# Kernel tuning notes

Hardware: AMD Instinct MI355X
Metric: run time of the kernel (lower is better)

## Reference

```python
import jax, jax.numpy as jnp
import numpy as np

N, E, B, IN, DIM, H = 20000, 320000, 128, 25, 64, 8

def _lin(key, fin, fout):
    k1, k2 = jax.random.split(key)
    s = 1.0 / np.sqrt(fin)
    return (jax.random.uniform(k1, (fin, fout), jnp.float32, -s, s),
            jax.random.uniform(k2, (fout,), jnp.float32, -s, s))

def setup_inputs() -> dict:
    key = jax.random.key(0)
    ks = jax.random.split(key, 12)
    x = jax.random.normal(ks[0], (N, IN), jnp.float32)
    edge_index = jax.random.randint(ks[1], (2, E), 0, N, jnp.int64)
    batch = jnp.sort(jax.random.randint(ks[2], (N,), 0, B, jnp.int64))
    W0, b0 = _lin(ks[3], IN, DIM)
    Wg, _ = _lin(ks[4], DIM, H * DIM)            # GATConv lin (no bias)
    att_src = jax.random.normal(ks[5], (H, DIM), jnp.float32) * (1.0 / np.sqrt(DIM))
    att_dst = jax.random.normal(ks[6], (H, DIM), jnp.float32) * (1.0 / np.sqrt(DIM))
    bg = jnp.zeros((H * DIM,), jnp.float32)       # GATConv output bias
    Wh, bh = _lin(ks[7], H * DIM, DIM)            # head_nn
    sl = 1.0 / np.sqrt(DIM)
    W_ih = jax.random.uniform(ks[8], (4 * DIM, 2 * DIM), jnp.float32, -sl, sl)
    W_hh = jax.random.uniform(ks[9], (4 * DIM, DIM), jnp.float32, -sl, sl)
    b_ih = jnp.zeros((4 * DIM,), jnp.float32)
    b_hh = jnp.zeros((4 * DIM,), jnp.float32)
    W1, b1 = _lin(ks[10], 2 * DIM, DIM)
    W2, b2 = _lin(ks[11], DIM, 1)
    return dict(x=x, edge_index=edge_index, batch=batch, W0=W0, b0=b0, Wg=Wg,
                att_src=att_src, att_dst=att_dst, bg=bg, Wh=Wh, bh=bh,
                W_ih=W_ih, W_hh=W_hh, b_ih=b_ih, b_hh=b_hh, W1=W1, b1=b1, W2=W2, b2=b2)

def _forward(x, edge_index, batch, W0, b0, Wg, att_src, att_dst, bg, Wh, bh,
             W_ih, W_hh, b_ih, b_hh, W1, b1, W2, b2):
    n = x.shape[0]
    h0 = jax.nn.relu(x @ W0 + b0)                         # [N, DIM]
    xh = (h0 @ Wg).reshape(n, H, DIM)                     # [N, H, C]
    # add self-loops (PyG GATConv default)
    loop = jnp.arange(n, dtype=edge_index.dtype)
    src = jnp.concatenate([edge_index[0], loop])
    dst = jnp.concatenate([edge_index[1], loop])
    a_s = jnp.einsum('nhc,hc->nh', xh, att_src)           # [N, H]
    a_d = jnp.einsum('nhc,hc->nh', xh, att_dst)
    e = jax.nn.leaky_relu(a_s[src] + a_d[dst], 0.2)       # [Etot, H]
    m = jax.ops.segment_max(e, dst, num_segments=n)
    w = jnp.exp(e - m[dst])
    s = jax.ops.segment_sum(w, dst, num_segments=n)
    alpha = w / s[dst]                                    # segment softmax over dst
    agg = jax.ops.segment_sum(alpha[:, :, None] * xh[src], dst, num_segments=n)
    out = jax.nn.relu(agg.reshape(n, H * DIM) + bg)
    out = jax.nn.relu(out @ Wh + bh)                      # [N, DIM]
    # Set2Set, 3 processing steps
    q_star = jnp.zeros((B, 2 * DIM), out.dtype)
    h = jnp.zeros((B, DIM), out.dtype)
    c = jnp.zeros((B, DIM), out.dtype)
    for _ in range(3):
        g = q_star @ W_ih.T + b_ih + h @ W_hh.T + b_hh
        i_g, f_g, g_g, o_g = jnp.split(g, 4, axis=-1)
        c = jax.nn.sigmoid(f_g) * c + jax.nn.sigmoid(i_g) * jnp.tanh(g_g)
        h = jax.nn.sigmoid(o_g) * jnp.tanh(c)
        q = h                                             # [B, DIM]
        e2 = jnp.sum(out * q[batch], axis=-1)             # [N]
        m2 = jax.ops.segment_max(e2, batch, num_segments=B)
        w2 = jnp.exp(e2 - m2[batch])
        s2 = jax.ops.segment_sum(w2, batch, num_segments=B)
        a2 = w2 / s2[batch]
        r = jax.ops.segment_sum(a2[:, None] * out, batch, num_segments=B)
        q_star = jnp.concatenate([q, r], axis=-1)
    y = jax.nn.relu(q_star @ W1 + b1)
    y = y @ W2 + b2
    return y.reshape(-1)

def reference(x, edge_index, batch, W0, b0, Wg, att_src, att_dst, bg, Wh, bh,
              W_ih, W_hh, b_ih, b_hh, W1, b1, W2, b2):
    return _forward(x, edge_index, batch, W0, b0, Wg, att_src, att_dst, bg, Wh, bh,
                    W_ih, W_hh, b_ih, b_hh, W1, b1, W2, b2)
```

## Files before the change

kernel.cpp:

```cpp
#include <hip/hip_runtime.h>

#define N_NODES 20000
#define N_EDGES 320000
#define NBATCH  128

__device__ __forceinline__ float lrelu(float v) { return v > 0.f ? v : 0.2f * v; }

__global__ void k_h0(const float* __restrict__ x, const float* __restrict__ W0,
                     const float* __restrict__ b0, float* __restrict__ h0,
                     int* __restrict__ deg, int n) {
    __shared__ float ws[25 * 64];
    __shared__ float bs[64];
    __shared__ float xs[100];
    int t = threadIdx.x;
    int gid = blockIdx.x * 256 + t;
    if (gid < n) deg[gid] = 0;
    for (int i = t; i < 25 * 64; i += 256) ws[i] = W0[i];
    if (t < 64) bs[t] = b0[t];
    int nb = blockIdx.x * 4;
    if (t < 100 && nb * 25 + t < n * 25) xs[t] = x[(size_t)nb * 25 + t];
    __syncthreads();
    int node = nb + (t >> 6);
    int c = t & 63;
    if (node >= n) return;
    float s = bs[c];
    const float* xr = xs + (t >> 6) * 25;
    #pragma unroll
    for (int k = 0; k < 25; k++) s += xr[k] * ws[k * 64 + c];
    h0[(size_t)node * 64 + c] = fmaxf(s, 0.f);
}

__global__ void k_small(const float* __restrict__ Wg, const float* __restrict__ att_s,
                        const float* __restrict__ att_d, float* __restrict__ vsd,
                        const int* __restrict__ batch, int* __restrict__ segst, int n, int b) {
    int t = threadIdx.x;
    if (blockIdx.x == 0) {
        int k = t >> 3, h = t & 7;
        const float* wrow = Wg + (size_t)k * 512 + h * 64;
        float s1 = 0.f, s2 = 0.f;
        #pragma unroll 8
        for (int c = 0; c < 64; c++) {
            float w = wrow[c];
            s1 += w * att_s[h * 64 + c];
            s2 += w * att_d[h * 64 + c];
        }
        vsd[k * 16 + h] = s1;
        vsd[k * 16 + 8 + h] = s2;
    } else {
        if (t > b) return;
        int lo = 0, hi = n;
        while (lo < hi) { int mid = (lo + hi) >> 1; if (batch[mid] < t) lo = mid + 1; else hi = mid; }
        segst[t] = lo;
    }
}

__global__ __launch_bounds__(256) void k_asd(const float* __restrict__ h0,
                                             const float* __restrict__ vsd,
                                             float* __restrict__ a_s, float* __restrict__ a_d) {
    __shared__ float hs[16][65];
    __shared__ float vl[64 * 16];
    int tid = threadIdx.x;
    int rbase = blockIdx.x * 16;
    {
        int row = tid / 16, c4 = (tid % 16) * 4;
        float4 hv = *(const float4*)(h0 + (size_t)(rbase + row) * 64 + c4);
        hs[row][c4] = hv.x; hs[row][c4 + 1] = hv.y; hs[row][c4 + 2] = hv.z; hs[row][c4 + 3] = hv.w;
    }
    #pragma unroll
    for (int j = 0; j < 4; j++) vl[tid + j * 256] = vsd[tid + j * 256];
    __syncthreads();
    int nl = tid / 16, o = tid % 16;
    float acc = 0.f;
    #pragma unroll 16
    for (int k = 0; k < 64; k++) acc += hs[nl][k] * vl[k * 16 + o];
    int node = rbase + nl;
    if (o < 8) a_s[node * 8 + o] = acc;
    else       a_d[node * 8 + (o - 8)] = acc;
}

__global__ void k_count(const int* __restrict__ dst, int* __restrict__ deg, int e) {
    int i = blockIdx.x * 256 + threadIdx.x;
    if (i < e) atomicAdd(&deg[dst[i]], 1);
}

__global__ __launch_bounds__(1024) void k_scan1(const int* __restrict__ deg,
                                                int* __restrict__ tmp, int* __restrict__ bsum, int n) {
    __shared__ int wsum[16];
    int tid = threadIdx.x, lane = tid & 63, w = tid >> 6;
    int i = blockIdx.x * 1024 + tid;
    int v = (i < n) ? deg[i] + 1 : 0;
    int x = v;
    #pragma unroll
    for (int off = 1; off < 64; off <<= 1) {
        int t = __shfl_up(x, off);
        if (lane >= off) x += t;
    }
    if (lane == 63) wsum[w] = x;
    __syncthreads();
    int pre = 0;
    #pragma unroll
    for (int j = 0; j < 16; j++) if (j < w) pre += wsum[j];
    if (i < n) tmp[i] = pre + x - v;
    if (tid == 1023) bsum[blockIdx.x] = pre + x;
}

__global__ void k_scan2(const int* __restrict__ tmp, const int* __restrict__ bsum,
                        const float* __restrict__ a_s, const float* __restrict__ a_d,
                        int* __restrict__ offs, int* __restrict__ adj,
                        int* __restrict__ cursor, float* __restrict__ eb, int n, int nblk) {
    int i = blockIdx.x * 256 + threadIdx.x;
    if (i > n) return;
    int b = i >> 10;
    int pre = 0;
    for (int j = 0; j < b; j++) pre += bsum[j];
    if (i == n) {
        int tot = pre;
        for (int j = b; j < nblk; j++) tot += bsum[j];
        offs[n] = tot;
        return;
    }
    int o = pre + tmp[i];
    offs[i] = o;
    adj[o] = i;
    cursor[i] = o + 1;
    float4 s0 = *(const float4*)(a_s + (size_t)i * 8);
    float4 s1 = *(const float4*)(a_s + (size_t)i * 8 + 4);
    float4 d0 = *(const float4*)(a_d + (size_t)i * 8);
    float4 d1 = *(const float4*)(a_d + (size_t)i * 8 + 4);
    float4 e0, e1;
    e0.x = lrelu(s0.x + d0.x); e0.y = lrelu(s0.y + d0.y);
    e0.z = lrelu(s0.z + d0.z); e0.w = lrelu(s0.w + d0.w);
    e1.x = lrelu(s1.x + d1.x); e1.y = lrelu(s1.y + d1.y);
    e1.z = lrelu(s1.z + d1.z); e1.w = lrelu(s1.w + d1.w);
    *(float4*)(eb + (size_t)o * 8) = e0;
    *(float4*)(eb + (size_t)o * 8 + 4) = e1;
}

__global__ void k_fill_edge(const int* __restrict__ src, const int* __restrict__ dst,
                            const float* __restrict__ a_s, const float* __restrict__ a_d,
                            int* __restrict__ cursor, int* __restrict__ adj,
                            float* __restrict__ eb, int e) {
    int i = blockIdx.x * 256 + threadIdx.x;
    if (i >= e) return;
    int s = src[i], d = dst[i];
    int p = atomicAdd(&cursor[d], 1);
    adj[p] = s;
    float4 s0 = *(const float4*)(a_s + (size_t)s * 8);
    float4 s1 = *(const float4*)(a_s + (size_t)s * 8 + 4);
    float4 d0 = *(const float4*)(a_d + (size_t)d * 8);
    float4 d1 = *(const float4*)(a_d + (size_t)d * 8 + 4);
    float4 e0, e1;
    e0.x = lrelu(s0.x + d0.x); e0.y = lrelu(s0.y + d0.y);
    e0.z = lrelu(s0.z + d0.z); e0.w = lrelu(s0.w + d0.w);
    e1.x = lrelu(s1.x + d1.x); e1.y = lrelu(s1.y + d1.y);
    e1.z = lrelu(s1.z + d1.z); e1.w = lrelu(s1.w + d1.w);
    *(float4*)(eb + (size_t)p * 8) = e0;
    *(float4*)(eb + (size_t)p * 8 + 4) = e1;
}

__global__ __launch_bounds__(256) void k_gat3(const int* __restrict__ offs, const int* __restrict__ adj,
                                              const float* __restrict__ eb,
                                              const float* __restrict__ h0,
                                              float* __restrict__ agg_pre, int n) {
    int lane = threadIdx.x & 63;
    int node = blockIdx.x * 4 + (threadIdx.x >> 6);
    if (node >= n) return;
    int beg = offs[node], end = offs[node + 1];
    int g = lane >> 3;

    float m = -1e30f, s = 0.f;
    for (int base = beg; base < end; base += 8) {
        if (base + g < end) {
            float ev = eb[(size_t)base * 8 + lane];
            if (ev > m) { s = s * __expf(m - ev) + 1.f; m = ev; }
            else        { s += __expf(ev - m); }
        }
    }
    #pragma unroll
    for (int off = 8; off < 64; off <<= 1) {
        float mo = __shfl_xor(m, off), so = __shfl_xor(s, off);
        float mn = fmaxf(m, mo);
        s = s * __expf(m - mn) + so * __expf(mo - mn);
        m = mn;
    }
    float rcp = 1.f / s;

    float acc[8] = {0.f, 0.f, 0.f, 0.f, 0.f, 0.f, 0.f, 0.f};
    for (int sbase = beg; sbase < end; sbase += 64) {
        int scnt = end - sbase; if (scnt > 64) scnt = 64;
        int srcv = 0;
        if (lane < scnt) srcv = adj[sbase + lane];
        float al[8];
        #pragma unroll
        for (int j = 0; j < 8; j++) {
            int q = j * 8 + g;
            float ev = -1e30f;
            if (q < scnt) ev = eb[(size_t)sbase * 8 + j * 64 + lane];
            al[j] = __expf(ev - m) * rcp;
        }
        for (int j = 0; j < 8; j++) {
            int qb = j * 8;
            if (qb >= scnt) break;
            int sg[8]; float xv[8];
            #pragma unroll
            for (int g2 = 0; g2 < 8; g2++) sg[g2] = __shfl(srcv, qb + g2);
            #pragma unroll
            for (int g2 = 0; g2 < 8; g2++)
                xv[g2] = h0[(size_t)sg[g2] * 64 + lane];
            #pragma unroll
            for (int g2 = 0; g2 < 8; g2++) {
                #pragma unroll
                for (int h2 = 0; h2 < 8; h2++)
                    acc[h2] += __shfl(al[j], g2 * 8 + h2) * xv[g2];
            }
        }
    }
    #pragma unroll
    for (int h2 = 0; h2 < 8; h2++)
        agg_pre[(size_t)node * 512 + h2 * 64 + lane] = acc[h2];
}

__global__ __launch_bounds__(256) void k_fused3(const float* __restrict__ agg_pre,
                                                const float* __restrict__ Wg,
                                                const float* __restrict__ bg,
                                                const float* __restrict__ Wh,
                                                float* __restrict__ part, int M) {
    __shared__ float As[64 * 68];
    __shared__ float Bs[64 * 64];
    __shared__ float Cs[64 * 68];
    int tid = threadIdx.x;
    int r0 = blockIdx.x * 64;
    int tx = tid % 16, ty = tid / 16;
    int rr = tid / 16, c4 = (tid % 16) * 4;
    float accO[4][4] = {};
    #pragma unroll
    for (int hh = 0; hh < 2; hh++) {
        int h = blockIdx.y * 2 + hh;
        #pragma unroll
        for (int pp = 0; pp < 4; pp++) {
            int r = rr + pp * 16;
            float4 av = make_float4(0.f, 0.f, 0.f, 0.f);
            if (r0 + r < M) av = *(const float4*)(agg_pre + (size_t)(r0 + r) * 512 + h * 64 + c4);
            *(float4*)&As[r * 68 + c4] = av;
            *(float4*)&Bs[r * 64 + c4] = *(const float4*)(Wg + (size_t)r * 512 + h * 64 + c4);
        }
        __syncthreads();
        float acc1[4][4] = {};
        #pragma unroll 4
        for (int kc = 0; kc < 16; kc++) {
            float4 b0 = *(const float4*)&Bs[(kc * 4 + 0) * 64 + tx * 4];
            float4 b1 = *(const float4*)&Bs[(kc * 4 + 1) * 64 + tx * 4];
            float4 b2 = *(const float4*)&Bs[(kc * 4 + 2) * 64 + tx * 4];
            float4 b3 = *(const float4*)&Bs[(kc * 4 + 3) * 64 + tx * 4];
            #pragma unroll
            for (int i = 0; i < 4; i++) {
                float4 a = *(const float4*)&As[(ty * 4 + i) * 68 + kc * 4];
                acc1[i][0] += a.x * b0.x + a.y * b1.x + a.z * b2.x + a.w * b3.x;
                acc1[i][1] += a.x * b0.y + a.y * b1.y + a.z * b2.y + a.w * b3.y;
                acc1[i][2] += a.x * b0.z + a.y * b1.z + a.z * b2.z + a.w * b3.z;
                acc1[i][3] += a.x * b0.w + a.y * b1.w + a.z * b2.w + a.w * b3.w;
            }
        }
        __syncthreads();
        float4 bgv = *(const float4*)(bg + h * 64 + tx * 4);
        #pragma unroll
        for (int i = 0; i < 4; i++) {
            float4 o;
            o.x = fmaxf(acc1[i][0] + bgv.x, 0.f);
            o.y = fmaxf(acc1[i][1] + bgv.y, 0.f);
            o.z = fmaxf(acc1[i][2] + bgv.z, 0.f);
            o.w = fmaxf(acc1[i][3] + bgv.w, 0.f);
            *(float4*)&Cs[(ty * 4 + i) * 68 + tx * 4] = o;
        }
        #pragma unroll
        for (int pp = 0; pp < 4; pp++) {
            int k = rr + pp * 16;
            *(float4*)&Bs[k * 64 + c4] = *(const float4*)(Wh + (size_t)(h * 64 + k) * 64 + c4);
        }
        __syncthreads();
        #pragma unroll 4
        for (int kc = 0; kc < 16; kc++) {
            float4 b0 = *(const float4*)&Bs[(kc * 4 + 0) * 64 + tx * 4];
            float4 b1 = *(const float4*)&Bs[(kc * 4 + 1) * 64 + tx * 4];
            float4 b2 = *(const float4*)&Bs[(kc * 4 + 2) * 64 + tx * 4];
            float4 b3 = *(const float4*)&Bs[(kc * 4 + 3) * 64 + tx * 4];
            #pragma unroll
            for (int i = 0; i < 4; i++) {
                float4 a = *(const float4*)&Cs[(ty * 4 + i) * 68 + kc * 4];
                accO[i][0] += a.x * b0.x + a.y * b1.x + a.z * b2.x + a.w * b3.x;
                accO[i][1] += a.x * b0.y + a.y * b1.y + a.z * b2.y + a.w * b3.y;
                accO[i][2] += a.x * b0.z + a.y * b1.z + a.z * b2.z + a.w * b3.z;
                accO[i][3] += a.x * b0.w + a.y * b1.w + a.z * b2.w + a.w * b3.w;
            }
        }
        __syncthreads();
    }
    float* Cb = part + (size_t)blockIdx.y * M * 64;
    #pragma unroll
    for (int i = 0; i < 4; i++) {
        int r = r0 + ty * 4 + i;
        if (r >= M) continue;
        float4 o;
        o.x = accO[i][0]; o.y = accO[i][1]; o.z = accO[i][2]; o.w = accO[i][3];
        *(float4*)(Cb + (size_t)r * 64 + tx * 4) = o;
    }
}

__global__ void k_reduce4(const float* __restrict__ part, const float* __restrict__ bias,
                          float* __restrict__ out, int M) {
    int idx = blockIdx.x * 256 + threadIdx.x;
    if (idx >= M * 16) return;
    int r = idx / 16, cq = idx % 16;
    float4 s = make_float4(0.f, 0.f, 0.f, 0.f);
    #pragma unroll
    for (int y = 0; y < 4; y++) {
        float4 p = *(const float4*)(part + ((size_t)y * M + r) * 64 + cq * 4);
        s.x += p.x; s.y += p.y; s.z += p.z; s.w += p.w;
    }
    float4 b = *(const float4*)(bias + cq * 4);
    s.x = fmaxf(s.x + b.x, 0.f); s.y = fmaxf(s.y + b.y, 0.f);
    s.z = fmaxf(s.z + b.z, 0.f); s.w = fmaxf(s.w + b.w, 0.f);
    *(float4*)(out + (size_t)r * 64 + cq * 4) = s;
}

#define SROWS 208
__global__ __launch_bounds__(256) void k_s2s(const float* __restrict__ out2,
                                             const int* __restrict__ segst,
                                             const float* __restrict__ W_ih, const float* __restrict__ W_hh,
                                             const float* __restrict__ b_ih, const float* __restrict__ b_hh,
                                             const float* __restrict__ W1, const float* __restrict__ b1,
                                             const float* __restrict__ W2, const float* __restrict__ b2,
                                             float* __restrict__ out) {
    int b = blockIdx.x, tid = threadIdx.x, lane = tid & 63, w = tid >> 6;
    __shared__ float sc[SROWS * 65];
    __shared__ float wlds[1024];
    __shared__ float hl[64], cl[64], rl[64];
    __shared__ float red[4];
    __shared__ float gsh[256];
    int beg = segst[b], end = segst[b + 1];
    int nrows = end - beg;
    int ncache = nrows < SROWS ? nrows : SROWS;
    for (int idx = tid; idx < ncache * 16; idx += 256) {
        int r = idx >> 4, q = idx & 15;
        float4 v = *(const float4*)(out2 + (size_t)(beg + r) * 64 + q * 4);
        float* p = &sc[r * 65 + q * 4];
        p[0] = v.x; p[1] = v.y; p[2] = v.z; p[3] = v.w;
    }
    if (tid < 64) { hl[tid] = 0.f; cl[tid] = 0.f; rl[tid] = 0.f; }
    __syncthreads();

    for (int it = 0; it < 3; it++) {
        {
            float acc = b_ih[tid] + b_hh[tid];
            const float* wi = W_ih + (size_t)tid * 128;
            const float* wh = W_hh + (size_t)tid * 64;
            #pragma unroll 8
            for (int k = 0; k < 64; k++) acc += hl[k] * (wi[k] + wh[k]) + rl[k] * wi[64 + k];
            gsh[tid] = acc;
        }
        __syncthreads();
        if (tid < 64) {
            float ig = gsh[tid], fg = gsh[64 + tid], gg = gsh[128 + tid], og = gsh[192 + tid];
            float cc = cl[tid];
            float si = 1.f / (1.f + __expf(-ig));
            float sf = 1.f / (1.f + __expf(-fg));
            float so = 1.f / (1.f + __expf(-og));
            float cn = sf * cc + si * tanhf(gg);
            cl[tid] = cn;
            hl[tid] = so * tanhf(cn);
        }
        __syncthreads();
        float ev[4];
        int nr = 0;
        float mloc = -1e30f;
        for (int i = tid; i < nrows; i += 256) {
            float d = 0.f;
            if (i < SROWS) {
                const float* rp = &sc[i * 65];
                #pragma unroll 16
                for (int j = 0; j < 64; j++) d += rp[j] * hl[j];
            } else {
                const float* rp = out2 + (size_t)(beg + i) * 64;
                for (int j = 0; j < 64; j++) d += rp[j] * hl[j];
            }
            ev[nr++] = d;
            mloc = fmaxf(mloc, d);
        }
        #pragma unroll
        for (int off = 1; off < 64; off <<= 1) mloc = fmaxf(mloc, __shfl_xor(mloc, off));
        if (lane == 0) red[w] = mloc;
        __syncthreads();
        float m = fmaxf(fmaxf(red[0], red[1]), fmaxf(red[2], red[3]));
        __syncthreads();
        float sloc = 0.f;
        nr = 0;
        for (int i = tid; i < nrows; i += 256) {
            float wv = __expf(ev[nr++] - m);
            if (i < 1024) wlds[i] = wv;
            sloc += wv;
        }
        #pragma unroll
        for (int off = 1; off < 64; off <<= 1) sloc += __shfl_xor(sloc, off);
        if (lane == 0) red[w] = sloc;
        __syncthreads();
        float sv = red[0] + red[1] + red[2] + red[3];
        float inv = sv > 0.f ? 1.f / sv : 0.f;
        float acc = 0.f;
        for (int i = w; i < nrows; i += 4) {
            float v = (i < SROWS) ? sc[i * 65 + lane] : out2[(size_t)(beg + i) * 64 + lane];
            acc += wlds[i] * v;
        }
        gsh[w * 64 + lane] = acc;
        __syncthreads();
        if (tid < 64)
            rl[tid] = (gsh[tid] + gsh[64 + tid] + gsh[128 + tid] + gsh[192 + tid]) * inv;
        __syncthreads();
    }
    if (tid < 64) {
        float t = b1[tid];
        #pragma unroll 8
        for (int k = 0; k < 64; k++)
            t += hl[k] * W1[(size_t)k * 64 + tid] + rl[k] * W1[(size_t)(64 + k) * 64 + tid];
        t = fmaxf(t, 0.f) * W2[tid];
        #pragma unroll
        for (int off = 32; off > 0; off >>= 1) t += __shfl_xor(t, off);
        if (tid == 0) out[b] = t + b2[0];
    }
}

extern "C" void kernel_launch(void* const* d_in, const int* in_sizes, int n_in,
                              void* d_out, int out_size, void* d_ws, size_t ws_size,
                              hipStream_t stream) {
    const float* x     = (const float*)d_in[0];
    const int*   ei    = (const int*)d_in[1];
    const int*   batch = (const int*)d_in[2];
    const float* W0    = (const float*)d_in[3];
    const float* b0    = (const float*)d_in[4];
    const float* Wg    = (const float*)d_in[5];
    const float* att_s = (const float*)d_in[6];
    const float* att_d = (const float*)d_in[7];
    const float* bg    = (const float*)d_in[8];
    const float* Wh    = (const float*)d_in[9];
    const float* bh    = (const float*)d_in[10];
    const float* W_ih  = (const float*)d_in[11];
    const float* W_hh  = (const float*)d_in[12];
    const float* b_ih  = (const float*)d_in[13];
    const float* b_hh  = (const float*)d_in[14];
    const float* W1    = (const float*)d_in[15];
    const float* b1    = (const float*)d_in[16];
    const float* W2    = (const float*)d_in[17];
    const float* b2    = (const float*)d_in[18];
    float* out = (float*)d_out;

    const int* esrc = ei;
    const int* edst = ei + N_EDGES;

    char* wsb = (char*)d_ws;
    size_t off = 0;
    auto alloc = [&](size_t bytes) {
        void* p = wsb + off;
        off = (off + bytes + 255) & ~(size_t)255;
        return p;
    };
    float* h0      = (float*)alloc((size_t)N_NODES * 64 * 4);
    float* agg_pre = (float*)alloc((size_t)N_NODES * 512 * 4);
    float* part    = (float*)alloc((size_t)4 * N_NODES * 64 * 4);
    float* out2    = (float*)alloc((size_t)N_NODES * 64 * 4);
    float* a_s     = (float*)alloc((size_t)N_NODES * 8 * 4);
    float* a_d     = (float*)alloc((size_t)N_NODES * 8 * 4);
    float* vsd     = (float*)alloc(64 * 16 * 4);
    float* eb      = (float*)alloc((size_t)(N_EDGES + N_NODES) * 8 * 4);
    int*   deg     = (int*)alloc((size_t)N_NODES * 4);
    int*   tmp     = (int*)alloc((size_t)N_NODES * 4);
    int*   bsum    = (int*)alloc(32 * 4);
    int*   offs    = (int*)alloc((size_t)(N_NODES + 1) * 4);
    int*   cursor  = (int*)alloc((size_t)N_NODES * 4);
    int*   adj     = (int*)alloc((size_t)(N_EDGES + N_NODES) * 4);
    int*   segst   = (int*)alloc((size_t)(NBATCH + 1) * 4);

    k_h0<<<(N_NODES + 3) / 4, 256, 0, stream>>>(x, W0, b0, h0, deg, N_NODES);
    k_small<<<2, 512, 0, stream>>>(Wg, att_s, att_d, vsd, batch, segst, N_NODES, NBATCH);
    k_asd<<<N_NODES / 16, 256, 0, stream>>>(h0, vsd, a_s, a_d);

    k_count<<<(N_EDGES + 255) / 256, 256, 0, stream>>>(edst, deg, N_EDGES);
    const int nblk = (N_NODES + 1023) / 1024;
    k_scan1<<<nblk, 1024, 0, stream>>>(deg, tmp, bsum, N_NODES);
    k_scan2<<<(N_NODES + 256) / 256, 256, 0, stream>>>(tmp, bsum, a_s, a_d, offs, adj, cursor, eb, N_NODES, nblk);
    k_fill_edge<<<(N_EDGES + 255) / 256, 256, 0, stream>>>(esrc, edst, a_s, a_d, cursor, adj, eb, N_EDGES);

    k_gat3<<<(N_NODES + 3) / 4, 256, 0, stream>>>(offs, adj, eb, h0, agg_pre, N_NODES);
    k_fused3<<<dim3((N_NODES + 63) / 64, 4), 256, 0, stream>>>(agg_pre, Wg, bg, Wh, part, N_NODES);
    k_reduce4<<<(N_NODES * 16 + 255) / 256, 256, 0, stream>>>(part, bh, out2, N_NODES);

    k_s2s<<<NBATCH, 256, 0, stream>>>(out2, segst, W_ih, W_hh, b_ih, b_hh, W1, b1, W2, b2, out);
}
```

Before: 310.4 us.

## Fuse partial-sum reduction into set2set and retile fused GEMM microkernel

Removes the k_reduce4 kernel and the out2 buffer. The set2set kernel now sums the four per-head-group partials, adds the bias and applies ReLU while it loads rows into shared memory (and on the uncached fallback path). The fused GEMM kernel changes its per-thread tile from 4x4 to 2x8 with outer-product accumulation and reuses one shared buffer for both the A and C tiles, which cuts LDS use. This saves a launch and a full write/read pass over the output, but the rows beyond the shared cache in s2s now read four partial buffers on every pass.

```diff
diff --git a/kernel.cpp b/kernel.cpp
--- a/kernel.cpp
+++ b/kernel.cpp
@@ -220,19 +220,19 @@
         agg_pre[(size_t)node * 512 + h2 * 64 + lane] = acc[h2];
 }
 
-__global__ __launch_bounds__(256) void k_fused3(const float* __restrict__ agg_pre,
+__global__ __launch_bounds__(256) void k_fused4(const float* __restrict__ agg_pre,
                                                 const float* __restrict__ Wg,
                                                 const float* __restrict__ bg,
                                                 const float* __restrict__ Wh,
                                                 float* __restrict__ part, int M) {
-    __shared__ float As[64 * 68];
+    __shared__ float AB[64 * 68];
     __shared__ float Bs[64 * 64];
-    __shared__ float Cs[64 * 68];
     int tid = threadIdx.x;
     int r0 = blockIdx.x * 64;
-    int tx = tid % 16, ty = tid / 16;
-    int rr = tid / 16, c4 = (tid % 16) * 4;
-    float accO[4][4] = {};
+    int tx = tid & 7;
+    int ty = tid >> 3;
+    int rr = tid >> 4, c4 = (tid & 15) * 4;
+    float4 accO[2][2] = {};
     #pragma unroll
     for (int hh = 0; hh < 2; hh++) {
         int h = blockIdx.y * 2 + hh;
@@ -241,36 +241,38 @@
             int r = rr + pp * 16;
             float4 av = make_float4(0.f, 0.f, 0.f, 0.f);
             if (r0 + r < M) av = *(const float4*)(agg_pre + (size_t)(r0 + r) * 512 + h * 64 + c4);
-            *(float4*)&As[r * 68 + c4] = av;
+            *(float4*)&AB[r * 68 + c4] = av;
             *(float4*)&Bs[r * 64 + c4] = *(const float4*)(Wg + (size_t)r * 512 + h * 64 + c4);
         }
         __syncthreads();
-        float acc1[4][4] = {};
+        float4 acc1[2][2] = {};
         #pragma unroll 4
         for (int kc = 0; kc < 16; kc++) {
-            float4 b0 = *(const float4*)&Bs[(kc * 4 + 0) * 64 + tx * 4];
-            float4 b1 = *(const float4*)&Bs[(kc * 4 + 1) * 64 + tx * 4];
-            float4 b2 = *(const float4*)&Bs[(kc * 4 + 2) * 64 + tx * 4];
-            float4 b3 = *(const float4*)&Bs[(kc * 4 + 3) * 64 + tx * 4];
+            float4 a0 = *(const float4*)&AB[(ty * 2 + 0) * 68 + kc * 4];
+            float4 a1 = *(const float4*)&AB[(ty * 2 + 1) * 68 + kc * 4];
             #pragma unroll
-            for (int i = 0; i < 4; i++) {
-                float4 a = *(const float4*)&As[(ty * 4 + i) * 68 + kc * 4];
-                acc1[i][0] += a.x * b0.x + a.y * b1.x + a.z * b2.x + a.w * b3.x;
-                acc1[i][1] += a.x * b0.y + a.y * b1.y + a.z * b2.y + a.w * b3.y;
-                acc1[i][2] += a.x * b0.z + a.y * b1.z + a.z * b2.z + a.w * b3.z;
-                acc1[i][3] += a.x * b0.w + a.y * b1.w + a.z * b2.w + a.w * b3.w;
+            for (int kk = 0; kk < 4; kk++) {
+                float ak0 = (&a0.x)[kk], ak1 = (&a1.x)[kk];
+                float4 bL = *(const float4*)&Bs[(kc * 4 + kk) * 64 + tx * 8];
+                float4 bH = *(const float4*)&Bs[(kc * 4 + kk) * 64 + tx * 8 + 4];
+                acc1[0][0].x += ak0 * bL.x; acc1[0][0].y += ak0 * bL.y; acc1[0][0].z += ak0 * bL.z; acc1[0][0].w += ak0 * bL.w;
+                acc1[0][1].x += ak0 * bH.x; acc1[0][1].y += ak0 * bH.y; acc1[0][1].z += ak0 * bH.z; acc1[0][1].w += ak0 * bH.w;
+                acc1[1][0].x += ak1 * bL.x; acc1[1][0].y += ak1 * bL.y; acc1[1][0].z += ak1 * bL.z; acc1[1][0].w += ak1 * bL.w;
+                acc1[1][1].x += ak1 * bH.x; acc1[1][1].y += ak1 * bH.y; acc1[1][1].z += ak1 * bH.z; acc1[1][1].w += ak1 * bH.w;
             }
         }
         __syncthreads();
-        float4 bgv = *(const float4*)(bg + h * 64 + tx * 4);
-        #pragma unroll
-        for (int i = 0; i < 4; i++) {
-            float4 o;
-            o.x = fmaxf(acc1[i][0] + bgv.x, 0.f);
-            o.y = fmaxf(acc1[i][1] + bgv.y, 0.f);
-            o.z = fmaxf(acc1[i][2] + bgv.z, 0.f);
-            o.w = fmaxf(acc1[i][3] + bgv.w, 0.f);
-            *(float4*)&Cs[(ty * 4 + i) * 68 + tx * 4] = o;
+        float4 bgL = *(const float4*)(bg + h * 64 + tx * 8);
+        float4 bgH = *(const float4*)(bg + h * 64 + tx * 8 + 4);
+        #pragma unroll
+        for (int i = 0; i < 2; i++) {
+            float4 cL, cH;
+            cL.x = fmaxf(acc1[i][0].x + bgL.x, 0.f); cL.y = fmaxf(acc1[i][0].y + bgL.y, 0.f);
+            cL.z = fmaxf(acc1[i][0].z + bgL.z, 0.f); cL.w = fmaxf(acc1[i][0].w + bgL.w, 0.f);
+            cH.x = fmaxf(acc1[i][1].x + bgH.x, 0.f); cH.y = fmaxf(acc1[i][1].y + bgH.y, 0.f);
+            cH.z = fmaxf(acc1[i][1].z + bgH.z, 0.f); cH.w = fmaxf(acc1[i][1].w + bgH.w, 0.f);
+            *(float4*)&AB[(ty * 2 + i) * 68 + tx * 8] = cL;
+            *(float4*)&AB[(ty * 2 + i) * 68 + tx * 8 + 4] = cH;
         }
         #pragma unroll
         for (int pp = 0; pp < 4; pp++) {
@@ -280,57 +282,40 @@
         __syncthreads();
         #pragma unroll 4
         for (int kc = 0; kc < 16; kc++) {
-            float4 b0 = *(const float4*)&Bs[(kc * 4 + 0) * 64 + tx * 4];
-            float4 b1 = *(const float4*)&Bs[(kc * 4 + 1) * 64 + tx * 4];
-            float4 b2 = *(const float4*)&Bs[(kc * 4 + 2) * 64 + tx * 4];
-            float4 b3 = *(const float4*)&Bs[(kc * 4 + 3) * 64 + tx * 4];
+            float4 a0 = *(const float4*)&AB[(ty * 2 + 0) * 68 + kc * 4];
+            float4 a1 = *(const float4*)&AB[(ty * 2 + 1) * 68 + kc * 4];
             #pragma unroll
-            for (int i = 0; i < 4; i++) {
-                float4 a = *(const float4*)&Cs[(ty * 4 + i) * 68 + kc * 4];
-                accO[i][0] += a.x * b0.x + a.y * b1.x + a.z * b2.x + a.w * b3.x;
-                accO[i][1] += a.x * b0.y + a.y * b1.y + a.z * b2.y + a.w * b3.y;
-                accO[i][2] += a.x * b0.z + a.y * b1.z + a.z * b2.z + a.w * b3.z;
-                accO[i][3] += a.x * b0.w + a.y * b1.w + a.z * b2.w + a.w * b3.w;
+            for (int kk = 0; kk < 4; kk++) {
+                float ak0 = (&a0.x)[kk], ak1 = (&a1.x)[kk];
+                float4 bL = *(const float4*)&Bs[(kc * 4 + kk) * 64 + tx * 8];
+                float4 bH = *(const float4*)&Bs[(kc * 4 + kk) * 64 + tx * 8 + 4];
+                accO[0][0].x += ak0 * bL.x; accO[0][0].y += ak0 * bL.y; accO[0][0].z += ak0 * bL.z; accO[0][0].w += ak0 * bL.w;
+                accO[0][1].x += ak0 * bH.x; accO[0][1].y += ak0 * bH.y; accO[0][1].z += ak0 * bH.z; accO[0][1].w += ak0 * bH.w;
+                accO[1][0].x += ak1 * bL.x; accO[1][0].y += ak1 * bL.y; accO[1][0].z += ak1 * bL.z; accO[1][0].w += ak1 * bL.w;
+                accO[1][1].x += ak1 * bH.x; accO[1][1].y += ak1 * bH.y; accO[1][1].z += ak1 * bH.z; accO[1][1].w += ak1 * bH.w;
             }
         }
         __syncthreads();
     }
     float* Cb = part + (size_t)blockIdx.y * M * 64;
     #pragma unroll
-    for (int i = 0; i < 4; i++) {
-        int r = r0 + ty * 4 + i;
+    for (int i = 0; i < 2; i++) {
+        int r = r0 + ty * 2 + i;
         if (r >= M) continue;
-        float4 o;
-        o.x = accO[i][0]; o.y = accO[i][1]; o.z = accO[i][2]; o.w = accO[i][3];
-        *(float4*)(Cb + (size_t)r * 64 + tx * 4) = o;
-    }
-}
-
-__global__ void k_reduce4(const float* __restrict__ part, const float* __restrict__ bias,
-                          float* __restrict__ out, int M) {
-    int idx = blockIdx.x * 256 + threadIdx.x;
-    if (idx >= M * 16) return;
-    int r = idx / 16, cq = idx % 16;
-    float4 s = make_float4(0.f, 0.f, 0.f, 0.f);
-    #pragma unroll
-    for (int y = 0; y < 4; y++) {
-        float4 p = *(const float4*)(part + ((size_t)y * M + r) * 64 + cq * 4);
-        s.x += p.x; s.y += p.y; s.z += p.z; s.w += p.w;
-    }
-    float4 b = *(const float4*)(bias + cq * 4);
-    s.x = fmaxf(s.x + b.x, 0.f); s.y = fmaxf(s.y + b.y, 0.f);
-    s.z = fmaxf(s.z + b.z, 0.f); s.w = fmaxf(s.w + b.w, 0.f);
-    *(float4*)(out + (size_t)r * 64 + cq * 4) = s;
+        *(float4*)(Cb + (size_t)r * 64 + tx * 8) = accO[i][0];
+        *(float4*)(Cb + (size_t)r * 64 + tx * 8 + 4) = accO[i][1];
+    }
 }
 
 #define SROWS 208
-__global__ __launch_bounds__(256) void k_s2s(const float* __restrict__ out2,
+__global__ __launch_bounds__(256) void k_s2s(const float* __restrict__ part,
+                                             const float* __restrict__ bh,
                                              const int* __restrict__ segst,
                                              const float* __restrict__ W_ih, const float* __restrict__ W_hh,
                                              const float* __restrict__ b_ih, const float* __restrict__ b_hh,
                                              const float* __restrict__ W1, const float* __restrict__ b1,
                                              const float* __restrict__ W2, const float* __restrict__ b2,
-                                             float* __restrict__ out) {
+                                             float* __restrict__ out, int M) {
     int b = blockIdx.x, tid = threadIdx.x, lane = tid & 63, w = tid >> 6;
     __shared__ float sc[SROWS * 65];
     __shared__ float wlds[1024];
@@ -340,11 +325,20 @@
     int beg = segst[b], end = segst[b + 1];
     int nrows = end - beg;
     int ncache = nrows < SROWS ? nrows : SROWS;
+    const size_t PS = (size_t)M * 64;
     for (int idx = tid; idx < ncache * 16; idx += 256) {
         int r = idx >> 4, q = idx & 15;
-        float4 v = *(const float4*)(out2 + (size_t)(beg + r) * 64 + q * 4);
+        const float* pb = part + (size_t)(beg + r) * 64 + q * 4;
+        float4 v0 = *(const float4*)pb;
+        float4 v1 = *(const float4*)(pb + PS);
+        float4 v2 = *(const float4*)(pb + 2 * PS);
+        float4 v3 = *(const float4*)(pb + 3 * PS);
+        float4 bv = *(const float4*)(bh + q * 4);
         float* p = &sc[r * 65 + q * 4];
-        p[0] = v.x; p[1] = v.y; p[2] = v.z; p[3] = v.w;
+        p[0] = fmaxf(v0.x + v1.x + v2.x + v3.x + bv.x, 0.f);
+        p[1] = fmaxf(v0.y + v1.y + v2.y + v3.y + bv.y, 0.f);
+        p[2] = fmaxf(v0.z + v1.z + v2.z + v3.z + bv.z, 0.f);
+        p[3] = fmaxf(v0.w + v1.w + v2.w + v3.w + bv.w, 0.f);
     }
     if (tid < 64) { hl[tid] = 0.f; cl[tid] = 0.f; rl[tid] = 0.f; }
     __syncthreads();
@@ -380,8 +374,11 @@
                 #pragma unroll 16
                 for (int j = 0; j < 64; j++) d += rp[j] * hl[j];
             } else {
-                const float* rp = out2 + (size_t)(beg + i) * 64;
-                for (int j = 0; j < 64; j++) d += rp[j] * hl[j];
+                const float* pb = part + (size_t)(beg + i) * 64;
+                for (int j = 0; j < 64; j++) {
+                    float v = pb[j] + pb[PS + j] + pb[2 * PS + j] + pb[3 * PS + j] + bh[j];
+                    d += fmaxf(v, 0.f) * hl[j];
+                }
             }
             ev[nr++] = d;
             mloc = fmaxf(mloc, d);
@@ -407,7 +404,12 @@
         float inv = sv > 0.f ? 1.f / sv : 0.f;
         float acc = 0.f;
         for (int i = w; i < nrows; i += 4) {
-            float v = (i < SROWS) ? sc[i * 65 + lane] : out2[(size_t)(beg + i) * 64 + lane];
+            float v;
+            if (i < SROWS) v = sc[i * 65 + lane];
+            else {
+                const float* pb = part + (size_t)(beg + i) * 64 + lane;
+                v = fmaxf(pb[0] + pb[PS] + pb[2 * PS] + pb[3 * PS] + bh[lane], 0.f);
+            }
             acc += wlds[i] * v;
         }
         gsh[w * 64 + lane] = acc;
@@ -465,7 +467,6 @@
     float* h0      = (float*)alloc((size_t)N_NODES * 64 * 4);
     float* agg_pre = (float*)alloc((size_t)N_NODES * 512 * 4);
     float* part    = (float*)alloc((size_t)4 * N_NODES * 64 * 4);
-    float* out2    = (float*)alloc((size_t)N_NODES * 64 * 4);
     float* a_s     = (float*)alloc((size_t)N_NODES * 8 * 4);
     float* a_d     = (float*)alloc((size_t)N_NODES * 8 * 4);
     float* vsd     = (float*)alloc(64 * 16 * 4);
@@ -489,8 +490,7 @@
     k_fill_edge<<<(N_EDGES + 255) / 256, 256, 0, stream>>>(esrc, edst, a_s, a_d, cursor, adj, eb, N_EDGES);
 
     k_gat3<<<(N_NODES + 3) / 4, 256, 0, stream>>>(offs, adj, eb, h0, agg_pre, N_NODES);
-    k_fused3<<<dim3((N_NODES + 63) / 64, 4), 256, 0, stream>>>(agg_pre, Wg, bg, Wh, part, N_NODES);
-    k_reduce4<<<(N_NODES * 16 + 255) / 256, 256, 0, stream>>>(part, bh, out2, N_NODES);
-
-    k_s2s<<<NBATCH, 256, 0, stream>>>(out2, segst, W_ih, W_hh, b_ih, b_hh, W1, b1, W2, b2, out);
-}
+    k_fused4<<<dim3((N_NODES + 63) / 64, 4), 256, 0, stream>>>(agg_pre, Wg, bg, Wh, part, N_NODES);
+
+    k_s2s<<<NBATCH, 256, 0, stream>>>(part, bh, segst, W_ih, W_hh, b_ih, b_hh, W1, b1, W2, b2, out, N_NODES);
+}
```

Result: faster. 294.5 us (-5.1%).
